# Performance work log

Hardware: AMD Instinct MI355X
Metric: run time of the kernel (lower is better)

## Reference

```python
import jax, jax.numpy as jnp
import numpy as np
import math

B, S, D = 1, 2048, 2048
H, KVH = 16, 8
HD = D // H                      # 128
M_, N_ = 8, 256                  # S = M_*N_ blocks of tokens
FH = 5632                        # multiple_of-rounded int(2*(4*D)/3)
EPS = 1e-6
THETA = 10000.0


def rmsnorm(x, w, eps=EPS):
    xf = x.astype(jnp.float32)
    y = xf * jax.lax.rsqrt(jnp.mean(xf * xf, axis=-1, keepdims=True) + eps)
    return y.astype(x.dtype) * w


def apply_rope(x, cos, sin):
    # x: (B, S, h, HD); cos/sin: (S, HD//2) -- consecutive-pair complex rotation
    x2 = x.reshape(*x.shape[:-1], HD // 2, 2)
    xr, xi = x2[..., 0], x2[..., 1]
    c = cos[None, :, None, :]
    s = sin[None, :, None, :]
    out = jnp.stack([xr * c - xi * s, xr * s + xi * c], axis=-1)
    return out.reshape(x.shape)


def setup_inputs() -> dict:
    key = jax.random.key(0)
    ks = jax.random.split(key, 12)
    sc = 0.02
    x = jax.random.normal(ks[0], (B, S, D), jnp.float32)
    vec = jax.random.normal(ks[1], (B, M_, D), jnp.float32)
    wq = jax.random.normal(ks[2], (D, H * HD), jnp.float32) * sc
    wk = jax.random.normal(ks[3], (D, KVH * HD), jnp.float32) * sc
    wv = jax.random.normal(ks[4], (D, KVH * HD), jnp.float32) * sc
    wo = jax.random.normal(ks[5], (H * HD, D), jnp.float32) * sc
    w1 = jax.random.normal(ks[6], (D, FH), jnp.float32) * sc
    w2 = jax.random.normal(ks[7], (FH, D), jnp.float32) * sc
    w3 = jax.random.normal(ks[8], (D, FH), jnp.float32) * sc
    mod_w = jax.random.normal(ks[9], (D, 3 * D), jnp.float32) * sc
    mod_b = jnp.zeros((3 * D,), jnp.float32)
    attn_norm_w = jnp.ones((D,), jnp.float32)
    ffn_norm_w = jnp.ones((D,), jnp.float32)
    # RoPE tables
    inv = 1.0 / (THETA ** (jnp.arange(0, HD, 2, dtype=jnp.float32) / HD))
    t = jnp.arange(S, dtype=jnp.float32)
    f = jnp.outer(t, inv)                      # (S, HD//2)
    cos, sin = jnp.cos(f), jnp.sin(f)
    mask = jnp.triu(jnp.full((S, S), -1e9, jnp.float32), 1)
    return dict(x=x, vec=vec, cos=cos, sin=sin, mask=mask, wq=wq, wk=wk, wv=wv,
                wo=wo, w1=w1, w2=w2, w3=w3, mod_w=mod_w, mod_b=mod_b,
                attn_norm_w=attn_norm_w, ffn_norm_w=ffn_norm_w)


def reference(x, vec, cos, sin, mask, wq, wk, wv, wo, w1, w2, w3,
              mod_w, mod_b, attn_norm_w, ffn_norm_w):
    n_rep = H // KVH
    # Modulation from per-block vectors (B, M, D) -> expand over N tokens/block
    mod = jax.nn.silu(vec) @ mod_w + mod_b
    shift, scale, gate = jnp.split(mod, 3, axis=-1)
    expand = lambda t: jnp.repeat(t, N_, axis=1)      # (B, M, D) -> (B, S, D)
    # Attention branch with modulated RMSNorm input
    h = rmsnorm(x, attn_norm_w)
    h = (1.0 + expand(scale)) * h + expand(shift)
    q = (h @ wq).reshape(B, S, H, HD)
    k = (h @ wk).reshape(B, S, KVH, HD)
    v = (h @ wv).reshape(B, S, KVH, HD)
    q = apply_rope(q, cos, sin)
    k = apply_rope(k, cos, sin)
    k = jnp.repeat(k, n_rep, axis=2)                  # repeat_kv
    v = jnp.repeat(v, n_rep, axis=2)
    scores = jnp.einsum('bshd,bthd->bhst', q, k) / math.sqrt(HD) + mask
    attn = jax.nn.softmax(scores.astype(jnp.float32), axis=-1).astype(q.dtype)
    o = jnp.einsum('bhst,bthd->bshd', attn, v).reshape(B, S, H * HD) @ wo
    x = x + expand(gate) * o
    # SwiGLU FFN branch
    hn = rmsnorm(x, ffn_norm_w)
    ff = (jax.nn.silu(hn @ w1) * (hn @ w3)) @ w2
    return x + ff
```

## Files before the change

### kernel.cpp

```cpp
#include <hip/hip_runtime.h>
#include <hip/hip_bf16.h>


typedef __attribute__((ext_vector_type(8))) short short8;
typedef __attribute__((ext_vector_type(4))) float f32x4;
typedef __attribute__((ext_vector_type(16))) float f32x16;
typedef __attribute__((ext_vector_type(4))) unsigned short u16x4;

#define MFMA16(a, b, c) __builtin_amdgcn_mfma_f32_16x16x32_bf16((a), (b), (c), 0, 0, 0)
#define MFMA32(a, b, c) __builtin_amdgcn_mfma_f32_32x32x16_bf16((a), (b), (c), 0, 0, 0)
#define VMCNT(n) asm volatile("s_waitcnt vmcnt(" #n ")" ::: "memory")

__device__ __forceinline__ unsigned short f2b_bits(float f) {
    union { float f; unsigned int u; } cv; cv.f = f;
    unsigned int u = cv.u;
    u += 0x7fffu + ((u >> 16) & 1u);
    return (unsigned short)(u >> 16);
}
__device__ __forceinline__ float b2f_bits(unsigned short b) {
    union { float f; unsigned int u; } cv; cv.u = ((unsigned int)b) << 16; return cv.f;
}
__device__ __forceinline__ float silu_f(float x) { return x / (1.0f + __expf(-x)); }

__device__ __forceinline__ void async_copy16(const unsigned short* g, unsigned short* l) {
    __builtin_amdgcn_global_load_lds(
        (const __attribute__((address_space(1))) unsigned int*)g,
        (__attribute__((address_space(3))) unsigned int*)l, 16, 0, 0);
}

__global__ __launch_bounds__(256) void transpose_kernel(
    const float* __restrict__ W, unsigned short* __restrict__ WT, int K, int N,
    float scale)
{
    __shared__ float t[64][65];
    const int tid = threadIdx.x;
    const int k0 = blockIdx.y * 64, n0 = blockIdx.x * 64;
    {
        const int row = tid >> 2, cq = (tid & 3) * 16;
        const float* src = W + (size_t)(k0 + row) * N + n0 + cq;
        #pragma unroll
        for (int i = 0; i < 4; i++) {
            float4 v = *(const float4*)(src + i * 4);
            t[row][cq + i * 4 + 0] = v.x;
            t[row][cq + i * 4 + 1] = v.y;
            t[row][cq + i * 4 + 2] = v.z;
            t[row][cq + i * 4 + 3] = v.w;
        }
    }
    __syncthreads();
    {
        const int n = tid >> 2, kq = (tid & 3) * 16;
        short8 v0, v1;
        #pragma unroll
        for (int i = 0; i < 8; i++) {
            v0[i] = (short)f2b_bits(t[kq + i][n] * scale);
            v1[i] = (short)f2b_bits(t[kq + 8 + i][n] * scale);
        }
        unsigned short* dst = WT + (size_t)(n0 + n) * K + k0 + kq;
        *(short8*)(dst) = v0;
        *(short8*)(dst + 8) = v1;
    }
}

__global__ __launch_bounds__(256) void transpose_w13_kernel(
    const float* __restrict__ W1, const float* __restrict__ W3,
    unsigned short* __restrict__ WT, int K, int N)
{
    __shared__ float t[64][65];
    const int tid = threadIdx.x;
    const int k0 = blockIdx.y * 64, n0 = blockIdx.x * 64;
    for (int which = 0; which < 2; which++) {
        const float* W = which ? W3 : W1;
        __syncthreads();
        {
            const int row = tid >> 2, cq = (tid & 3) * 16;
            const float* src = W + (size_t)(k0 + row) * N + n0 + cq;
            #pragma unroll
            for (int i = 0; i < 4; i++) {
                float4 v = *(const float4*)(src + i * 4);
                t[row][cq + i * 4 + 0] = v.x;
                t[row][cq + i * 4 + 1] = v.y;
                t[row][cq + i * 4 + 2] = v.z;
                t[row][cq + i * 4 + 3] = v.w;
            }
        }
        __syncthreads();
        {
            const int n = tid >> 2, kq = (tid & 3) * 16;
            short8 v0, v1;
            #pragma unroll
            for (int i = 0; i < 8; i++) {
                v0[i] = (short)f2b_bits(t[kq + i][n]);
                v1[i] = (short)f2b_bits(t[kq + 8 + i][n]);
            }
            const int ngl = n0 + n;
            const int r = ((ngl >> 3) << 4) + (ngl & 7) + which * 8;
            unsigned short* dst = WT + (size_t)r * K + k0 + kq;
            *(short8*)(dst) = v0;
            *(short8*)(dst + 8) = v1;
        }
    }
}

__global__ void silu_kernel(const float* __restrict__ in, float* __restrict__ outp, int n) {
    int i = blockIdx.x * 256 + threadIdx.x;
    if (i < n) outp[i] = silu_f(i < n ? in[i] : 0.0f);
}

__global__ __launch_bounds__(256) void mod_gemm1(
    const float* __restrict__ svec, const float* __restrict__ mw,
    float* __restrict__ part)
{
    __shared__ float svs[8][256];
    const int tid = threadIdx.x;
    const int nb = blockIdx.x, kc = blockIdx.y;
    const int n = nb * 256 + tid;
    #pragma unroll
    for (int m8 = 0; m8 < 8; m8++) svs[m8][tid] = svec[m8 * 2048 + kc * 256 + tid];
    __syncthreads();
    float acc[8];
    #pragma unroll
    for (int m = 0; m < 8; m++) acc[m] = 0.0f;
    for (int k = 0; k < 256; k++) {
        const float w = mw[(size_t)(kc * 256 + k) * 6144 + n];
        #pragma unroll
        for (int m = 0; m < 8; m++) acc[m] += svs[m][k] * w;
    }
    #pragma unroll
    for (int m = 0; m < 8; m++) part[(size_t)(kc * 8 + m) * 6144 + n] = acc[m];
}

__global__ void mod_gemm2(const float* __restrict__ part, const float* __restrict__ mb,
                          float* __restrict__ modb)
{
    const int i = blockIdx.x * 256 + threadIdx.x;
    const int n = i % 6144;
    float a = mb[n];
    #pragma unroll
    for (int kc = 0; kc < 8; kc++) a += part[(size_t)(kc * 8 + (i / 6144)) * 6144 + n];
    modb[i] = a;
}

template<bool MOD>
__global__ __launch_bounds__(256) void norm_kernel(
    const float* __restrict__ xin, const float* __restrict__ w,
    const float* __restrict__ mod, unsigned short* __restrict__ outp)
{
    const int s = blockIdx.x, tid = threadIdx.x;
    const float* xr = xin + (size_t)s * 2048;
    float4 a4 = *(const float4*)(xr + tid * 8);
    float4 b4 = *(const float4*)(xr + tid * 8 + 4);
    float v[8] = {a4.x, a4.y, a4.z, a4.w, b4.x, b4.y, b4.z, b4.w};
    float ss = 0.0f;
    #pragma unroll
    for (int i = 0; i < 8; i++) ss += v[i] * v[i];
    #pragma unroll
    for (int off = 1; off < 64; off <<= 1) ss += __shfl_xor(ss, off);
    __shared__ float red[4];
    if ((tid & 63) == 0) red[tid >> 6] = ss;
    __syncthreads();
    ss = red[0] + red[1] + red[2] + red[3];
    const float inv = rsqrtf(ss * (1.0f / 2048.0f) + 1e-6f);
    const int g = s >> 8;
    #pragma unroll
    for (int i = 0; i < 8; i++) {
        const int d = tid * 8 + i;
        float y = v[i] * inv * w[d];
        if (MOD) y = y * (1.0f + mod[g * 6144 + 2048 + d]) + mod[g * 6144 + d];
        outp[(size_t)s * 2048 + d] = f2b_bits(y);
    }
}

enum { EP_QKV = 0 };

template<int EPI>
__global__ __launch_bounds__(256, 2) void gemm_kernel(
    const unsigned short* __restrict__ A, const unsigned short* __restrict__ BT,
    void* __restrict__ outp, void* __restrict__ outp2, void* __restrict__ outp3,
    const float* __restrict__ ct, const float* __restrict__ st,
    int M, int N, int K)
{
    __shared__ unsigned short As[8192];
    __shared__ unsigned short Bs[8192];
    const int tid = threadIdx.x;
    const int lane = tid & 63, wave = tid >> 6;

    const int nwg = gridDim.x * gridDim.y;
    const int fid = blockIdx.y * gridDim.x + blockIdx.x;
    const int sid = (fid & 7) * (nwg >> 3) + (fid >> 3);
    const int m0 = (sid / gridDim.x) * 128;
    const int n0 = (sid % gridDim.x) * 128;

    const int wr = (wave >> 1) * 64, wc = (wave & 1) * 64;
    const int lr = lane & 15, lg = lane >> 4;
    const int rcol = (lg ^ ((lr >> 1) & 3)) * 8;

    const int cl0 = (wave * 2 + 0) * 64 + lane;
    const int cl1 = (wave * 2 + 1) * 64 + lane;
    const int r0 = cl0 >> 2, c0 = cl0 & 3;
    const int r1 = cl1 >> 2, c1 = cl1 & 3;
    const unsigned short* gA0 = A + (size_t)(m0 + r0) * K + (c0 ^ ((r0 >> 1) & 3)) * 8;
    const unsigned short* gA1 = A + (size_t)(m0 + r1) * K + (c1 ^ ((r1 >> 1) & 3)) * 8;
    const unsigned short* gB0 = BT + (size_t)(n0 + r0) * K + (c0 ^ ((r0 >> 1) & 3)) * 8;
    const unsigned short* gB1 = BT + (size_t)(n0 + r1) * K + (c1 ^ ((r1 >> 1) & 3)) * 8;

    f32x4 acc[4][4];
    #pragma unroll
    for (int i = 0; i < 4; i++)
        #pragma unroll
        for (int j = 0; j < 4; j++) acc[i][j] = (f32x4){0.f, 0.f, 0.f, 0.f};

    const int nsteps = K >> 5;

    auto stage = [&](int buf, int kofs) {
        unsigned short* la = As + buf * 4096 + wave * 1024;
        unsigned short* lb = Bs + buf * 4096 + wave * 1024;
        async_copy16(gA0 + kofs, la);
        async_copy16(gA1 + kofs, la + 512);
        async_copy16(gB0 + kofs, lb);
        async_copy16(gB1 + kofs, lb + 512);
    };
    auto dostep = [&](int t, int cur) {
        if (t + 1 < nsteps) stage(cur ^ 1, (t + 1) * 32);
        const unsigned short* ab = As + cur * 4096;
        const unsigned short* bb = Bs + cur * 4096;
        short8 af[4], bfr[4];
        #pragma unroll
        for (int i = 0; i < 4; i++)
            af[i] = *(const short8*)&ab[(wr + i * 16 + lr) * 32 + rcol];
        #pragma unroll
        for (int j = 0; j < 4; j++)
            bfr[j] = *(const short8*)&bb[(wc + j * 16 + lr) * 32 + rcol];
        #pragma unroll
        for (int i = 0; i < 4; i++)
            #pragma unroll
            for (int j = 0; j < 4; j++)
                acc[i][j] = MFMA16(af[i], bfr[j], acc[i][j]);
        __syncthreads();
    };

    stage(0, 0);
    __syncthreads();
    for (int t = 0; t < nsteps; t += 2) { dostep(t, 0); dostep(t + 1, 1); }

    #pragma unroll
    for (int i = 0; i < 4; i++) {
        #pragma unroll
        for (int j = 0; j < 4; j++) {
            const int rb = m0 + wr + i * 16 + lg * 4;
            const int c  = n0 + wc + j * 16 + lr;
            if (n0 < 3072) {
                const int crel = (n0 < 2048) ? c : (c - 2048);
                const int dd = crel & 127;
                const int pr = dd >> 1;
                #pragma unroll
                for (int r = 0; r < 4; r++) {
                    const float v = acc[i][j][r];
                    const float p = __shfl_xor(v, 1);
                    const float cs = ct[(rb + r) * 64 + pr];
                    const float sn = st[(rb + r) * 64 + pr];
                    const float res = (dd & 1) ? (p * sn + v * cs) : (v * cs - p * sn);
                    if (n0 < 2048)
                        ((unsigned short*)outp)[(size_t)(rb + r) * 2048 + crel] = f2b_bits(res);
                    else
                        ((unsigned short*)outp2)[(size_t)(rb + r) * 1024 + crel] = f2b_bits(res);
                }
            } else {
                u16x4 pk4;
                #pragma unroll
                for (int r = 0; r < 4; r++) pk4[r] = f2b_bits(acc[i][j][r]);
                *(u16x4*)((unsigned short*)outp3 + (size_t)(c - 3072) * 2048 + rb) = pk4;
            }
        }
    }
}

enum { G_SILU = 0, G_PART = 1 };

template<int EPI>
__global__ __launch_bounds__(512, 1) void gemm256_kernel(
    const unsigned short* __restrict__ A, const unsigned short* __restrict__ BT,
    void* __restrict__ outp, int M, int N, int Nout, int K, int ktiles, int nsplit)
{
    extern __shared__ unsigned short smem[];
    unsigned short* As_ = smem;
    unsigned short* Bs_ = smem + 2 * 16384;
    const int tid = threadIdx.x;
    const int lane = tid & 63, wid = tid >> 6;
    const int wm = wid >> 2, wn = wid & 3;
    const int lr = lane & 15, lg = lane >> 4;

    const int nwg = gridDim.x * gridDim.y;
    const int fid = blockIdx.y * gridDim.x + blockIdx.x;
    const int sid = (fid & 7) * (nwg >> 3) + (fid >> 3);
    const int m0 = (sid / gridDim.x) * 256;
    const int n0 = (sid % gridDim.x) * 256;
    const int z = blockIdx.z;
    const int kt0 = (z * ktiles) / nsplit;
    const int nt = ((z + 1) * ktiles) / nsplit - kt0;

    const int srow8 = wid * 8 + (lane >> 3);
    const int schunk = lane & 7;

    f32x4 acc[8][4];
    #pragma unroll
    for (int i = 0; i < 8; i++)
        #pragma unroll
        for (int j = 0; j < 4; j++) acc[i][j] = (f32x4){0.f, 0.f, 0.f, 0.f};

    auto stageA = [&](int u, int t) {
        const int row = u * 64 + srow8;
        async_copy16(A + (size_t)(m0 + row) * K + (size_t)(kt0 + t) * 64
                       + ((schunk ^ (row & 7)) << 3),
                     As_ + (t & 1) * 16384 + (u * 64 + wid * 8) * 64);
    };
    auto stageB = [&](int u, int t) {
        const int row = u * 64 + srow8;
        async_copy16(BT + (size_t)(n0 + row) * K + (size_t)(kt0 + t) * 64
                       + ((schunk ^ (row & 7)) << 3),
                     Bs_ + (t & 1) * 16384 + (u * 64 + wid * 8) * 64);
    };

    short8 areg[4], breg[2][4];
    auto loadA = [&](const unsigned short* ab, int mh, int ks) {
        #pragma unroll
        for (int i = 0; i < 4; i++) {
            const int row = wm * 128 + mh * 64 + i * 16 + lr;
            areg[i] = *(const short8*)&ab[row * 64 + (((ks * 4 + lg) ^ (row & 7)) << 3)];
        }
    };
    auto loadB = [&](const unsigned short* bb, int ks) {
        #pragma unroll
        for (int nj = 0; nj < 4; nj++) {
            const int row = wn * 64 + nj * 16 + lr;
            breg[ks][nj] = *(const short8*)&bb[row * 64 + (((ks * 4 + lg) ^ (row & 7)) << 3)];
        }
    };
    auto mmac = [&](int mh, int ks) {
        #pragma unroll
        for (int i = 0; i < 4; i++)
            #pragma unroll
            for (int nj = 0; nj < 4; nj++)
                acc[mh * 4 + i][nj] = MFMA16(areg[i], breg[ks][nj], acc[mh * 4 + i][nj]);
    };

    stageA(0, 0); stageA(2, 0);
    stageB(0, 0); stageB(1, 0);
    stageB(2, 0); stageB(3, 0);
    stageA(1, 0); stageA(3, 0);
    VMCNT(2);
    __builtin_amdgcn_sched_barrier(0);
    __builtin_amdgcn_s_barrier();
    __builtin_amdgcn_sched_barrier(0);

    for (int t = 0; t < nt; ++t) {
        const unsigned short* ab = As_ + (t & 1) * 16384;
        const unsigned short* bb = Bs_ + (t & 1) * 16384;
        const bool more = (t + 1 < nt);
        loadB(bb, 0);
        loadA(ab, 0, 0);
        if (more) { stageA(0, t + 1); stageA(2, t + 1); }
        __builtin_amdgcn_s_barrier();
        __builtin_amdgcn_s_setprio(1);
        mmac(0, 0);
        __builtin_amdgcn_s_setprio(0);
        __builtin_amdgcn_s_barrier();
        loadB(bb, 1);
        loadA(ab, 0, 1);
        if (more) { stageB(0, t + 1); stageB(1, t + 1); }
        __builtin_amdgcn_s_barrier();
        __builtin_amdgcn_s_setprio(1);
        mmac(0, 1);
        __builtin_amdgcn_s_setprio(0);
        if (more) { VMCNT(4); } else { VMCNT(0); }
        __builtin_amdgcn_sched_barrier(0);
        __builtin_amdgcn_s_barrier();
        __builtin_amdgcn_sched_barrier(0);
        loadA(ab, 1, 0);
        if (more) { stageB(2, t + 1); stageB(3, t + 1); }
        __builtin_amdgcn_s_barrier();
        __builtin_amdgcn_s_setprio(1);
        mmac(1, 0);
        __builtin_amdgcn_s_setprio(0);
        __builtin_amdgcn_s_barrier();
        loadA(ab, 1, 1);
        if (more) { stageA(1, t + 1); stageA(3, t + 1); }
        __builtin_amdgcn_s_barrier();
        __builtin_amdgcn_s_setprio(1);
        mmac(1, 1);
        __builtin_amdgcn_s_setprio(0);
        if (more) { VMCNT(2); __builtin_amdgcn_sched_barrier(0); }
        __builtin_amdgcn_s_barrier();
        __builtin_amdgcn_sched_barrier(0);
    }

    #pragma unroll
    for (int mi = 0; mi < 8; mi++) {
        #pragma unroll
        for (int nj = 0; nj < 4; nj++) {
            const int rb = m0 + wm * 128 + mi * 16 + lg * 4;
            const int c  = n0 + wn * 64 + nj * 16 + lr;
            if constexpr (EPI == G_SILU) {
                const int oc = ((c - lr) >> 1) + lr;
                #pragma unroll
                for (int r = 0; r < 4; r++) {
                    const float v = acc[mi][nj][r];
                    const float p = __shfl_xor(v, 8);
                    if (lr < 8)
                        ((unsigned short*)outp)[(size_t)(rb + r) * Nout + oc] =
                            f2b_bits(silu_f(v) * p);
                }
            } else {
                float* pout = (float*)outp + (size_t)z * M * Nout;
                #pragma unroll
                for (int r = 0; r < 4; r++)
                    pout[(size_t)(rb + r) * Nout + c] = acc[mi][nj][r];
            }
        }
    }
}

__global__ void combine_xgate(const float* __restrict__ p, const float* __restrict__ x,
                              const float* __restrict__ modp, float* __restrict__ out)
{
    const size_t i = ((size_t)blockIdx.x * 256 + threadIdx.x) * 4;
    const int row = (int)(i >> 11), col = (int)(i & 2047);
    const float4 a = *(const float4*)(p + i);
    const float4 b = *(const float4*)(p + (size_t)2048 * 2048 + i);
    const float4 xv = *(const float4*)(x + i);
    const float4 g = *(const float4*)(modp + (row >> 8) * 6144 + 4096 + col);
    float4 o;
    o.x = xv.x + g.x * (a.x + b.x);
    o.y = xv.y + g.y * (a.y + b.y);
    o.z = xv.z + g.z * (a.z + b.z);
    o.w = xv.w + g.w * (a.w + b.w);
    *(float4*)(out + i) = o;
}

__global__ void combine_w2(const float* __restrict__ p, float* __restrict__ out)
{
    const size_t i = ((size_t)blockIdx.x * 256 + threadIdx.x) * 4;
    const float4 a = *(const float4*)(p + i);
    const float4 b = *(const float4*)(p + (size_t)2048 * 2048 + i);
    const float4 c = *(const float4*)(p + (size_t)2 * 2048 * 2048 + i);
    float4 o = *(const float4*)(out + i);
    o.x += a.x + b.x + c.x; o.y += a.y + b.y + c.y;
    o.z += a.z + b.z + c.z; o.w += a.w + b.w + c.w;
    *(float4*)(out + i) = o;
}

__global__ __launch_bounds__(256, 2) void attn_kernel(
    const unsigned short* __restrict__ q,
    const unsigned short* __restrict__ kk,
    const unsigned short* __restrict__ vT,
    unsigned short* __restrict__ o)
{
    __shared__ unsigned short Ks[2][8192];
    __shared__ unsigned short Vs[2][8192];
    const int tid = threadIdx.x, wave = tid >> 6, lane = tid & 63;
    const int l5 = lane & 31, hi = lane >> 5;
    const int kvh = blockIdx.x;
    const int qt  = 63 - blockIdx.y;
    const int hs = wave >> 1, ks = wave & 1;
    const int h = kvh * 2 + hs;
    const int q0 = qt * 32;
    const int qrow = q0 + l5;
    const int niter = (qt >> 1) + 1;
    const int nss = (niter + 1) >> 1;

    short8 qf[8];
    {
        const unsigned short* qp = q + (size_t)qrow * 2048 + h * 128 + hi * 8;
        #pragma unroll
        for (int kf = 0; kf < 8; kf++) qf[kf] = *(const short8*)(qp + kf * 16);
    }

    f32x16 ot[4];
    #pragma unroll
    for (int df = 0; df < 4; df++)
        #pragma unroll
        for (int r = 0; r < 16; r++) ot[df][r] = 0.0f;
    float m_ = -3e30f, l_ = 0.0f;

    for (int ss = 0; ss < nss; ss++) {
        const int kvA = ss * 128;
        #pragma unroll
        for (int t = 0; t < 2; t++) {
            #pragma unroll
            for (int i = 0; i < 4; i++) {
                const int cl = (wave * 4 + i) * 64 + lane;
                const int row = cl >> 4, c = cl & 15;
                async_copy16(kk + (size_t)(kvA + t * 64 + row) * 1024 + kvh * 128
                                 + ((c ^ (row & 15)) * 8),
                             &Ks[t][(wave * 4 + i) * 512]);
            }
            #pragma unroll
            for (int i = 0; i < 4; i++) {
                const int cl = (wave * 4 + i) * 64 + lane;
                const int row = cl >> 3, c = cl & 7;
                async_copy16(vT + (size_t)(kvh * 128 + row) * 2048 + kvA + t * 64
                                 + ((c ^ (row & 7)) * 8),
                             &Vs[t][(wave * 4 + i) * 512]);
            }
        }
        __syncthreads();

        const int j = 2 * ss + ks;
        if (j < niter) {
            const int kv0 = j * 64;
            f32x16 st_[2];
            #pragma unroll
            for (int nf = 0; nf < 2; nf++)
                #pragma unroll
                for (int r = 0; r < 16; r++) st_[nf][r] = 0.0f;
            #pragma unroll
            for (int kf = 0; kf < 8; kf++) {
                const int ch = (kf * 2 + hi) ^ (l5 & 15);
                const short8 k0v = *(const short8*)&Ks[ks][l5 * 128 + ch * 8];
                const short8 k1v = *(const short8*)&Ks[ks][(l5 + 32) * 128 + ch * 8];
                st_[0] = MFMA32(k0v, qf[kf], st_[0]);
                st_[1] = MFMA32(k1v, qf[kf], st_[1]);
            }
            float sv[2][16];
            #pragma unroll
            for (int nf = 0; nf < 2; nf++)
                #pragma unroll
                for (int r = 0; r < 16; r++) {
                    const int kvi = kv0 + nf * 32 + (r & 3) + 8 * (r >> 2) + 4 * hi;
                    sv[nf][r] = (kvi > qrow) ? -3e30f : st_[nf][r];
                }
            float pmax = sv[0][0];
            #pragma unroll
            for (int nf = 0; nf < 2; nf++)
                #pragma unroll
                for (int r = 0; r < 16; r++) pmax = fmaxf(pmax, sv[nf][r]);
            pmax = fmaxf(pmax, __shfl_xor(pmax, 32));
            const float mnew = fmaxf(m_, pmax);
            const float alpha = __expf(m_ - mnew);
            m_ = mnew;
            float rs = 0.0f;
            #pragma unroll
            for (int nf = 0; nf < 2; nf++)
                #pragma unroll
                for (int r = 0; r < 16; r++) {
                    const float p = __expf(sv[nf][r] - mnew);
                    sv[nf][r] = p;
                    rs += p;
                }
            rs += __shfl_xor(rs, 32);
            l_ = l_ * alpha + rs;
            #pragma unroll
            for (int df = 0; df < 4; df++)
                #pragma unroll
                for (int r = 0; r < 16; r++) ot[df][r] *= alpha;
            short8 pa[4];
            #pragma unroll
            for (int nf = 0; nf < 2; nf++) {
                #pragma unroll
                for (int hh = 0; hh < 2; hh++) {
                    unsigned int a0 = ((unsigned int)f2b_bits(sv[nf][8 * hh + 1]) << 16) | f2b_bits(sv[nf][8 * hh + 0]);
                    unsigned int a1 = ((unsigned int)f2b_bits(sv[nf][8 * hh + 3]) << 16) | f2b_bits(sv[nf][8 * hh + 2]);
                    unsigned int a2 = ((unsigned int)f2b_bits(sv[nf][8 * hh + 5]) << 16) | f2b_bits(sv[nf][8 * hh + 4]);
                    unsigned int a3 = ((unsigned int)f2b_bits(sv[nf][8 * hh + 7]) << 16) | f2b_bits(sv[nf][8 * hh + 6]);
                    const unsigned int x0 = (unsigned int)__shfl_xor((int)a0, 32);
                    const unsigned int x1 = (unsigned int)__shfl_xor((int)a1, 32);
                    const unsigned int x2 = (unsigned int)__shfl_xor((int)a2, 32);
                    const unsigned int x3 = (unsigned int)__shfl_xor((int)a3, 32);
                    union { unsigned int u[4]; short8 s; } cv;
                    cv.u[0] = hi ? x2 : a0;
                    cv.u[1] = hi ? x3 : a1;
                    cv.u[2] = hi ? a2 : x0;
                    cv.u[3] = hi ? a3 : x1;
                    pa[nf * 2 + hh] = cv.s;
                }
            }
            #pragma unroll
            for (int df = 0; df < 4; df++) {
                const int d = df * 32 + l5;
                #pragma unroll
                for (int kvf = 0; kvf < 4; kvf++) {
                    const int ch = (kvf * 2 + hi) ^ (d & 7);
                    const short8 vfrag = *(const short8*)&Vs[ks][d * 64 + ch * 8];
                    ot[df] = MFMA32(vfrag, pa[kvf], ot[df]);
                }
            }
        }
        __syncthreads();
    }

    float* Osh = (float*)&Ks[0][0];
    float* msh = (float*)&Vs[0][0];
    if (ks == 1) {
        #pragma unroll
        for (int df = 0; df < 4; df++)
            #pragma unroll
            for (int r = 0; r < 16; r++) {
                const int d = df * 32 + (r & 3) + 8 * (r >> 2) + 4 * hi;
                Osh[hs * 4096 + d * 32 + l5] = ot[df][r];
            }
        if (hi == 0) { msh[hs * 64 + l5] = m_; msh[hs * 64 + 32 + l5] = l_; }
    }
    __syncthreads();
    if (ks == 0) {
        const float m1 = msh[hs * 64 + l5], l1 = msh[hs * 64 + 32 + l5];
        const float mF = fmaxf(m_, m1);
        const float a0 = __expf(m_ - mF), a1 = __expf(m1 - mF);
        const float rinv = 1.0f / (l_ * a0 + l1 * a1);
        #pragma unroll
        for (int df = 0; df < 4; df++) {
            #pragma unroll
            for (int g = 0; g < 4; g++) {
                u16x4 pk;
                #pragma unroll
                for (int e = 0; e < 4; e++) {
                    const int d = df * 32 + e + 8 * g + 4 * hi;
                    const float ov = ot[df][4 * g + e] * a0 + Osh[hs * 4096 + d * 32 + l5] * a1;
                    pk[e] = f2b_bits(ov * rinv);
                }
                *(u16x4*)(o + (size_t)qrow * 2048 + h * 128 + df * 32 + 8 * g + 4 * hi) = pk;
            }
        }
    }
}

extern "C" void kernel_launch(void* const* d_in, const int* in_sizes, int n_in,
                              void* d_out, int out_size, void* d_ws, size_t ws_size,
                              hipStream_t stream) {
    (void)in_sizes; (void)n_in; (void)out_size; (void)ws_size;
    const float* x     = (const float*)d_in[0];
    const float* vec   = (const float*)d_in[1];
    const float* cosb  = (const float*)d_in[2];
    const float* sinb  = (const float*)d_in[3];
    const float* wq    = (const float*)d_in[5];
    const float* wk    = (const float*)d_in[6];
    const float* wv    = (const float*)d_in[7];
    const float* wo    = (const float*)d_in[8];
    const float* w1    = (const float*)d_in[9];
    const float* w2    = (const float*)d_in[10];
    const float* w3    = (const float*)d_in[11];
    const float* mod_w = (const float*)d_in[12];
    const float* mod_b = (const float*)d_in[13];
    const float* anw   = (const float*)d_in[14];
    const float* fnw   = (const float*)d_in[15];
    float* out = (float*)d_out;

    char* ws = (char*)d_ws;
    size_t off = 0;
    auto alloc = [&](size_t bytes) -> void* {
        void* p = ws + off; off += (bytes + 255) & ~(size_t)255; return p;
    };
    unsigned short* WTqkv = (unsigned short*)alloc((size_t)4096 * 2048 * 2);
    unsigned short* WTo   = (unsigned short*)alloc((size_t)2048 * 2048 * 2);
    unsigned short* WT13  = (unsigned short*)alloc((size_t)11264 * 2048 * 2);
    unsigned short* WT2   = (unsigned short*)alloc((size_t)2048 * 5632 * 2);
    float* svec = (float*)alloc((size_t)8 * 2048 * 4);
    float* part = (float*)alloc((size_t)64 * 6144 * 4);
    float* modb = (float*)alloc((size_t)8 * 6144 * 4);
    unsigned short* h    = (unsigned short*)alloc((size_t)2048 * 2048 * 2);
    unsigned short* qb   = (unsigned short*)alloc((size_t)2048 * 2048 * 2);
    unsigned short* kb   = (unsigned short*)alloc((size_t)2048 * 1024 * 2);
    unsigned short* vT   = (unsigned short*)alloc((size_t)1024 * 2048 * 2);
    unsigned short* ob   = (unsigned short*)alloc((size_t)2048 * 2048 * 2);
    unsigned short* u    = (unsigned short*)alloc((size_t)2048 * 5632 * 2);
    unsigned short* ffin = (unsigned short*)alloc((size_t)2048 * 5632 * 2);

    float* pxg = (float*)u;
    float* pw2 = (float*)h;

    const float qscale = 0.08838834764831845f;

    hipFuncSetAttribute((const void*)gemm256_kernel<G_SILU>,
                        hipFuncAttributeMaxDynamicSharedMemorySize, 131072);
    hipFuncSetAttribute((const void*)gemm256_kernel<G_PART>,
                        hipFuncAttributeMaxDynamicSharedMemorySize, 131072);

    transpose_kernel<<<dim3(32, 32), 256, 0, stream>>>(wq, WTqkv, 2048, 2048, qscale);
    transpose_kernel<<<dim3(16, 32), 256, 0, stream>>>(wk, WTqkv + (size_t)2048 * 2048, 2048, 1024, 1.0f);
    transpose_kernel<<<dim3(16, 32), 256, 0, stream>>>(wv, WTqkv + (size_t)3072 * 2048, 2048, 1024, 1.0f);
    transpose_kernel<<<dim3(32, 32), 256, 0, stream>>>(wo, WTo, 2048, 2048, 1.0f);
    transpose_w13_kernel<<<dim3(88, 32), 256, 0, stream>>>(w1, w3, WT13, 2048, 5632);
    transpose_kernel<<<dim3(32, 88), 256, 0, stream>>>(w2, WT2, 5632, 2048, 1.0f);

    silu_kernel<<<64, 256, 0, stream>>>(vec, svec, 8 * 2048);
    mod_gemm1<<<dim3(24, 8), 256, 0, stream>>>(svec, mod_w, part);
    mod_gemm2<<<192, 256, 0, stream>>>(part, mod_b, modb);

    norm_kernel<true><<<2048, 256, 0, stream>>>(x, anw, modb, h);

    gemm_kernel<EP_QKV><<<dim3(32, 16), 256, 0, stream>>>(
        h, WTqkv, qb, kb, vT, cosb, sinb, 2048, 4096, 2048);

    attn_kernel<<<dim3(8, 64), 256, 0, stream>>>(qb, kb, vT, ob);

    gemm256_kernel<G_PART><<<dim3(8, 8, 2), 512, 131072, stream>>>(
        ob, WTo, pxg, 2048, 2048, 2048, 2048, 32, 2);
    combine_xgate<<<4096, 256, 0, stream>>>(pxg, x, modb, out);

    norm_kernel<false><<<2048, 256, 0, stream>>>(out, fnw, nullptr, h);

    gemm256_kernel<G_SILU><<<dim3(44, 8, 1), 512, 131072, stream>>>(
        h, WT13, ffin, 2048, 11264, 5632, 2048, 32, 1);

    gemm256_kernel<G_PART><<<dim3(8, 8, 3), 512, 131072, stream>>>(
        ffin, WT2, pw2, 2048, 2048, 2048, 5632, 88, 3);
    combine_w2<<<4096, 256, 0, stream>>>(pw2, out);
}
```

Baseline: 468.3 us.

## Switch 256x256 GEMM to four-stage pipeline with K=32 tiles

Restructures the large bf16 GEMM mainloop. It moves from a double-buffered K=64 tile to a four-slot ring of K=32 tiles, prefetching three tiles ahead with a graded vmcnt wait near the tail. A new 2-bit XOR swizzle replaces the old 3-bit one for LDS bank conflicts, and each iteration needs fewer barriers. The aim is to hide global-load latency more deeply; the cost is less MFMA work per barrier and twice as many loop iterations. A trivial redundant bounds check in the silu kernel is also dropped.

```diff
diff --git a/kernel.cpp b/kernel.cpp
--- a/kernel.cpp
+++ b/kernel.cpp
@@ -104,7 +104,7 @@
 
 __global__ void silu_kernel(const float* __restrict__ in, float* __restrict__ outp, int n) {
     int i = blockIdx.x * 256 + threadIdx.x;
-    if (i < n) outp[i] = silu_f(i < n ? in[i] : 0.0f);
+    if (i < n) outp[i] = silu_f(in[i]);
 }
 
 __global__ __launch_bounds__(256) void mod_gemm1(
@@ -284,7 +284,7 @@
 {
     extern __shared__ unsigned short smem[];
     unsigned short* As_ = smem;
-    unsigned short* Bs_ = smem + 2 * 16384;
+    unsigned short* Bs_ = smem + 4 * 8192;
     const int tid = threadIdx.x;
     const int lane = tid & 63, wid = tid >> 6;
     const int wm = wid >> 2, wn = wid & 3;
@@ -299,97 +299,79 @@
     const int kt0 = (z * ktiles) / nsplit;
     const int nt = ((z + 1) * ktiles) / nsplit - kt0;
 
-    const int srow8 = wid * 8 + (lane >> 3);
-    const int schunk = lane & 7;
-
     f32x4 acc[8][4];
     #pragma unroll
     for (int i = 0; i < 8; i++)
         #pragma unroll
         for (int j = 0; j < 4; j++) acc[i][j] = (f32x4){0.f, 0.f, 0.f, 0.f};
 
+    const int srow = wid * 16 + (lane >> 2);
+    const int sch  = (lane & 3) ^ ((srow >> 1) & 3);
     auto stageA = [&](int u, int t) {
-        const int row = u * 64 + srow8;
-        async_copy16(A + (size_t)(m0 + row) * K + (size_t)(kt0 + t) * 64
-                       + ((schunk ^ (row & 7)) << 3),
-                     As_ + (t & 1) * 16384 + (u * 64 + wid * 8) * 64);
+        const int row = u * 128 + srow;
+        async_copy16(A + (size_t)(m0 + row) * K + (size_t)(kt0 + t) * 32 + sch * 8,
+                     As_ + (t & 3) * 8192 + (u * 128 + wid * 16) * 32);
     };
     auto stageB = [&](int u, int t) {
-        const int row = u * 64 + srow8;
-        async_copy16(BT + (size_t)(n0 + row) * K + (size_t)(kt0 + t) * 64
-                       + ((schunk ^ (row & 7)) << 3),
-                     Bs_ + (t & 1) * 16384 + (u * 64 + wid * 8) * 64);
-    };
-
-    short8 areg[4], breg[2][4];
-    auto loadA = [&](const unsigned short* ab, int mh, int ks) {
+        const int row = u * 128 + srow;
+        async_copy16(BT + (size_t)(n0 + row) * K + (size_t)(kt0 + t) * 32 + sch * 8,
+                     Bs_ + (t & 3) * 8192 + (u * 128 + wid * 16) * 32);
+    };
+
+    short8 areg[4], breg[4];
+    auto loadA = [&](const unsigned short* ab, int mh) {
         #pragma unroll
         for (int i = 0; i < 4; i++) {
             const int row = wm * 128 + mh * 64 + i * 16 + lr;
-            areg[i] = *(const short8*)&ab[row * 64 + (((ks * 4 + lg) ^ (row & 7)) << 3)];
-        }
-    };
-    auto loadB = [&](const unsigned short* bb, int ks) {
+            areg[i] = *(const short8*)&ab[row * 32 + ((lg ^ ((row >> 1) & 3)) << 3)];
+        }
+    };
+    auto loadB = [&](const unsigned short* bb) {
         #pragma unroll
         for (int nj = 0; nj < 4; nj++) {
             const int row = wn * 64 + nj * 16 + lr;
-            breg[ks][nj] = *(const short8*)&bb[row * 64 + (((ks * 4 + lg) ^ (row & 7)) << 3)];
-        }
-    };
-    auto mmac = [&](int mh, int ks) {
+            breg[nj] = *(const short8*)&bb[row * 32 + ((lg ^ ((row >> 1) & 3)) << 3)];
+        }
+    };
+    auto mmac = [&](int mh) {
         #pragma unroll
         for (int i = 0; i < 4; i++)
             #pragma unroll
             for (int nj = 0; nj < 4; nj++)
-                acc[mh * 4 + i][nj] = MFMA16(areg[i], breg[ks][nj], acc[mh * 4 + i][nj]);
-    };
-
-    stageA(0, 0); stageA(2, 0);
-    stageB(0, 0); stageB(1, 0);
-    stageB(2, 0); stageB(3, 0);
-    stageA(1, 0); stageA(3, 0);
-    VMCNT(2);
+                acc[mh * 4 + i][nj] = MFMA16(areg[i], breg[nj], acc[mh * 4 + i][nj]);
+    };
+
+    stageA(0, 0); stageA(1, 0); stageB(0, 0); stageB(1, 0);
+    stageA(0, 1); stageA(1, 1); stageB(0, 1); stageB(1, 1);
+    stageA(0, 2); stageA(1, 2); stageB(0, 2); stageB(1, 2);
+    VMCNT(8);
     __builtin_amdgcn_sched_barrier(0);
     __builtin_amdgcn_s_barrier();
     __builtin_amdgcn_sched_barrier(0);
 
     for (int t = 0; t < nt; ++t) {
-        const unsigned short* ab = As_ + (t & 1) * 16384;
-        const unsigned short* bb = Bs_ + (t & 1) * 16384;
-        const bool more = (t + 1 < nt);
-        loadB(bb, 0);
-        loadA(ab, 0, 0);
-        if (more) { stageA(0, t + 1); stageA(2, t + 1); }
+        const unsigned short* ab = As_ + (t & 3) * 8192;
+        const unsigned short* bb = Bs_ + (t & 3) * 8192;
+        const bool more = (t + 3 < nt);
+        loadB(bb);
+        loadA(ab, 0);
+        if (more) { stageA(0, t + 3); stageA(1, t + 3); }
         __builtin_amdgcn_s_barrier();
         __builtin_amdgcn_s_setprio(1);
-        mmac(0, 0);
+        mmac(0);
         __builtin_amdgcn_s_setprio(0);
         __builtin_amdgcn_s_barrier();
-        loadB(bb, 1);
-        loadA(ab, 0, 1);
-        if (more) { stageB(0, t + 1); stageB(1, t + 1); }
+        loadA(ab, 1);
+        if (more) { stageB(0, t + 3); stageB(1, t + 3); }
         __builtin_amdgcn_s_barrier();
         __builtin_amdgcn_s_setprio(1);
-        mmac(0, 1);
+        mmac(1);
         __builtin_amdgcn_s_setprio(0);
-        if (more) { VMCNT(4); } else { VMCNT(0); }
+        const int rem = nt - 1 - t;
+        if (rem >= 3)      { VMCNT(8); }
+        else if (rem == 2) { VMCNT(4); }
+        else if (rem == 1) { VMCNT(0); }
         __builtin_amdgcn_sched_barrier(0);
-        __builtin_amdgcn_s_barrier();
-        __builtin_amdgcn_sched_barrier(0);
-        loadA(ab, 1, 0);
-        if (more) { stageB(2, t + 1); stageB(3, t + 1); }
-        __builtin_amdgcn_s_barrier();
-        __builtin_amdgcn_s_setprio(1);
-        mmac(1, 0);
-        __builtin_amdgcn_s_setprio(0);
-        __builtin_amdgcn_s_barrier();
-        loadA(ab, 1, 1);
-        if (more) { stageA(1, t + 1); stageA(3, t + 1); }
-        __builtin_amdgcn_s_barrier();
-        __builtin_amdgcn_s_setprio(1);
-        mmac(1, 1);
-        __builtin_amdgcn_s_setprio(0);
-        if (more) { VMCNT(2); __builtin_amdgcn_sched_barrier(0); }
         __builtin_amdgcn_s_barrier();
         __builtin_amdgcn_sched_barrier(0);
     }
@@ -693,15 +675,15 @@
     attn_kernel<<<dim3(8, 64), 256, 0, stream>>>(qb, kb, vT, ob);
 
     gemm256_kernel<G_PART><<<dim3(8, 8, 2), 512, 131072, stream>>>(
-        ob, WTo, pxg, 2048, 2048, 2048, 2048, 32, 2);
+        ob, WTo, pxg, 2048, 2048, 2048, 2048, 64, 2);
     combine_xgate<<<4096, 256, 0, stream>>>(pxg, x, modb, out);
 
     norm_kernel<false><<<2048, 256, 0, stream>>>(out, fnw, nullptr, h);
 
     gemm256_kernel<G_SILU><<<dim3(44, 8, 1), 512, 131072, stream>>>(
-        h, WT13, ffin, 2048, 11264, 5632, 2048, 32, 1);
+        h, WT13, ffin, 2048, 11264, 5632, 2048, 64, 1);
 
     gemm256_kernel<G_PART><<<dim3(8, 8, 3), 512, 131072, stream>>>(
-        ffin, WT2, pw2, 2048, 2048, 2048, 5632, 88, 3);
+        ffin, WT2, pw2, 2048, 2048, 2048, 5632, 176, 3);
     combine_w2<<<4096, 256, 0, stream>>>(pw2, out);
 }
```

After: 475.8 us. Within noise of the previous version (+1.6%).
